# Kernel optimization log

Measured on AMD Instinct MI355X. Metric: run time of the kernel, lower is better.

Reference implementation:

```python
import jax, jax.numpy as jnp
import numpy as np

TAU = 2.0
V_TH = 1.0
V_RESET = 0.0
BN_EPS = 1e-5
SG_ALPHA = 2.0  # spikingjelly ATan surrogate default

@jax.custom_vjp
def spike_fn(x):
    return (x >= 0.0).astype(x.dtype)

def _spike_fwd(x):
    return spike_fn(x), x

def _spike_bwd(x, g):
    # ATan surrogate: alpha/2 / (1 + (pi/2*alpha*x)^2)
    sg = (SG_ALPHA / 2.0) / (1.0 + (jnp.pi / 2.0 * SG_ALPHA * x) ** 2)
    return (g * sg,)

spike_fn.defvjp(_spike_fwd, _spike_bwd)

def lif_multistep(x_seq):
    # x_seq: [T, B, C]; decay_input=False, hard reset, detach_reset=True
    def step(v, xt):
        v = v - (v - V_RESET) / TAU + xt
        s = spike_fn(v - V_TH)
        sd = jax.lax.stop_gradient(s)
        v = (1.0 - sd) * v + sd * V_RESET
        return v, s
    v0 = jnp.zeros_like(x_seq[0])
    _, s_seq = jax.lax.scan(step, v0, x_seq)
    return s_seq

def bn_eval(x, gamma, beta, mean, var):
    # x: [T, B, C], normalize over channel C (eval-mode BN)
    inv = gamma * jax.lax.rsqrt(var + BN_EPS)
    return x * inv + (beta - mean * inv)

def setup_inputs() -> dict:
    key = jax.random.key(0)
    ks = jax.random.split(key, 8)
    B, T, Cin, C, K = 64, 200, 80, 1024, 7
    x = jax.random.normal(ks[0], (B, T, Cin), dtype=jnp.float32)
    pw_w = jax.random.normal(ks[1], (C, Cin), dtype=jnp.float32) * (1.0 / np.sqrt(Cin))
    pw_b = jnp.zeros((C,), dtype=jnp.float32)
    dw_w = jax.random.normal(ks[2], (C, K), dtype=jnp.float32) * (1.0 / np.sqrt(K))
    dw_b = jnp.zeros((C,), dtype=jnp.float32)
    bn1_gamma = jnp.ones((C,), dtype=jnp.float32)
    bn1_beta = jnp.zeros((C,), dtype=jnp.float32)
    bn1_mean = jnp.zeros((C,), dtype=jnp.float32)
    bn1_var = jnp.ones((C,), dtype=jnp.float32)
    lin_w = jax.random.normal(ks[3], (C, C), dtype=jnp.float32) * (1.0 / np.sqrt(C))
    bn2_gamma = jnp.ones((C,), dtype=jnp.float32)
    bn2_beta = jnp.zeros((C,), dtype=jnp.float32)
    bn2_mean = jnp.zeros((C,), dtype=jnp.float32)
    bn2_var = jnp.ones((C,), dtype=jnp.float32)
    return dict(x=x, pw_w=pw_w, pw_b=pw_b, dw_w=dw_w, dw_b=dw_b,
                bn1_gamma=bn1_gamma, bn1_beta=bn1_beta, bn1_mean=bn1_mean, bn1_var=bn1_var,
                lin_w=lin_w,
                bn2_gamma=bn2_gamma, bn2_beta=bn2_beta, bn2_mean=bn2_mean, bn2_var=bn2_var)

def reference(x, pw_w, pw_b, dw_w, dw_b,
              bn1_gamma, bn1_beta, bn1_mean, bn1_var,
              lin_w,
              bn2_gamma, bn2_beta, bn2_mean, bn2_var):
    # x: [B, T, Cin] -> trans1 -> [B, Cin, T]
    h = jnp.transpose(x, (0, 2, 1))
    # pointwise conv1d (kernel 1): [B, Cin, T] -> [B, C, T]
    h = jnp.einsum('bct,oc->bot', h, pw_w) + pw_b[None, :, None]
    # depthwise conv1d, kernel 7, same padding
    C = dw_w.shape[0]
    h = jax.lax.conv_general_dilated(
        h, dw_w[:, None, :], window_strides=(1,), padding=[(3, 3)],
        feature_group_count=C, dimension_numbers=('NCH', 'OIH', 'NCH'))
    h = h + dw_b[None, :, None]
    # trans2: [B, C, T] -> [T, B, C]
    h = jnp.transpose(h, (2, 0, 1))
    h = bn_eval(h, bn1_gamma, bn1_beta, bn1_mean, bn1_var)
    h = lif_multistep(h)
    # dropout1: eval mode -> identity
    h_res = h
    h = jnp.einsum('tbc,oc->tbo', h, lin_w)  # Linear, no bias
    h = bn_eval(h, bn2_gamma, bn2_beta, bn2_mean, bn2_var)
    h = lif_multistep(h)
    # dropout2: eval mode -> identity
    return h + h_res  # [T, B, C]
```

## Files before the change

kernel.cpp:

```cpp
#include <hip/hip_runtime.h>
#include <hip/hip_bf16.h>
#include <stdint.h>

#define B_    64
#define T_    200
#define CIN_  80
#define C_    1024
#define M_    (B_ * T_)
#define BCEL  (B_ * C_)

typedef __attribute__((ext_vector_type(4))) float f32x4;
typedef __attribute__((ext_vector_type(8))) _Float16 f16x8;
typedef __attribute__((ext_vector_type(4))) unsigned int u32x4;

__global__ __launch_bounds__(256) void gemm_abt128(
    const float* __restrict__ A, const float* __restrict__ Bm,
    const float* __restrict__ bias, float* __restrict__ C,
    int M, int N, int K) {
  __shared__ float As[16][128];
  __shared__ float Bs[16][128];
  const int tid = threadIdx.x;
  const int tx = tid & 15;
  const int ty = tid >> 4;
  const int m0 = blockIdx.x * 128;
  const int n0 = blockIdx.y * 128;
  const int lr = tid >> 1;
  const int lc = (tid & 1) * 8;

  float acc[8][8] = {};

  const float* Ar = A + (size_t)(m0 + lr) * K + lc;
  const float* Br = Bm + (size_t)(n0 + lr) * K + lc;

  float4 a0 = *(const float4*)(Ar + 0);
  float4 a1 = *(const float4*)(Ar + 4);
  float4 b0 = *(const float4*)(Br + 0);
  float4 b1 = *(const float4*)(Br + 4);

  for (int k0 = 0; k0 < K; k0 += 16) {
    __syncthreads();
    As[lc + 0][lr] = a0.x; As[lc + 1][lr] = a0.y;
    As[lc + 2][lr] = a0.z; As[lc + 3][lr] = a0.w;
    As[lc + 4][lr] = a1.x; As[lc + 5][lr] = a1.y;
    As[lc + 6][lr] = a1.z; As[lc + 7][lr] = a1.w;
    Bs[lc + 0][lr] = b0.x; Bs[lc + 1][lr] = b0.y;
    Bs[lc + 2][lr] = b0.z; Bs[lc + 3][lr] = b0.w;
    Bs[lc + 4][lr] = b1.x; Bs[lc + 5][lr] = b1.y;
    Bs[lc + 6][lr] = b1.z; Bs[lc + 7][lr] = b1.w;
    __syncthreads();
    if (k0 + 16 < K) {
      a0 = *(const float4*)(Ar + k0 + 16);
      a1 = *(const float4*)(Ar + k0 + 20);
      b0 = *(const float4*)(Br + k0 + 16);
      b1 = *(const float4*)(Br + k0 + 20);
    }
#pragma unroll
    for (int kk = 0; kk < 16; ++kk) {
      float4 av0 = *(const float4*)&As[kk][ty * 4];
      float4 av1 = *(const float4*)&As[kk][ty * 4 + 64];
      float4 bv0 = *(const float4*)&Bs[kk][tx * 4];
      float4 bv1 = *(const float4*)&Bs[kk][tx * 4 + 64];
      float avv[8] = {av0.x, av0.y, av0.z, av0.w, av1.x, av1.y, av1.z, av1.w};
      float bvv[8] = {bv0.x, bv0.y, bv0.z, bv0.w, bv1.x, bv1.y, bv1.z, bv1.w};
#pragma unroll
      for (int i = 0; i < 8; ++i)
#pragma unroll
        for (int j = 0; j < 8; ++j)
          acc[i][j] = fmaf(avv[i], bvv[j], acc[i][j]);
    }
  }

  float bj[8] = {0.f, 0.f, 0.f, 0.f, 0.f, 0.f, 0.f, 0.f};
  if (bias) {
#pragma unroll
    for (int j = 0; j < 8; ++j)
      bj[j] = bias[n0 + tx * 4 + (j & 3) + (j >> 2) * 64];
  }
#pragma unroll
  for (int i = 0; i < 8; ++i) {
    int row = m0 + ty * 4 + (i & 3) + (i >> 2) * 64;
    float4 o0, o1;
    o0.x = acc[i][0] + bj[0]; o0.y = acc[i][1] + bj[1];
    o0.z = acc[i][2] + bj[2]; o0.w = acc[i][3] + bj[3];
    o1.x = acc[i][4] + bj[4]; o1.y = acc[i][5] + bj[5];
    o1.z = acc[i][6] + bj[6]; o1.w = acc[i][7] + bj[7];
    *(float4*)&C[(size_t)row * N + n0 + tx * 4] = o0;
    *(float4*)&C[(size_t)row * N + n0 + tx * 4 + 64] = o1;
  }
}

__global__ __launch_bounds__(256) void dw_bn_lif(
    const float* __restrict__ p, const float* __restrict__ dw_w,
    const float* __restrict__ dw_b, const float* __restrict__ gam,
    const float* __restrict__ bet, const float* __restrict__ mu,
    const float* __restrict__ var, ushort* __restrict__ s1) {
  int gid = blockIdx.x * blockDim.x + threadIdx.x;
  int b = gid >> 10;
  int o = gid & 1023;

  float w[7];
#pragma unroll
  for (int k = 0; k < 7; ++k) w[k] = dw_w[o * 7 + k];
  float db = dw_b[o];
  float inv = (float)((double)gam[o] / sqrt((double)var[o] + 1e-5));
  float add = (float)((double)bet[o] - (double)mu[o] * (double)inv);

  const float* pp = p + (size_t)b * T_ * C_ + o;
  float win[14];
  win[0] = 0.f; win[1] = 0.f; win[2] = 0.f;
#pragma unroll
  for (int i = 0; i < 11; ++i) win[3 + i] = pp[(size_t)i * C_];

  float v = 0.f;
  size_t obase = (size_t)b * C_ + o;
  for (int c = 0; c < T_ / 8; ++c) {
    int t0 = c * 8;
    float nx[8];
#pragma unroll
    for (int j = 0; j < 8; ++j) {
      int tn = t0 + 11 + j;
      nx[j] = (tn < T_) ? pp[(size_t)tn * C_] : 0.f;
    }
#pragma unroll
    for (int s = 0; s < 8; ++s) {
      float u = db;
#pragma unroll
      for (int k = 0; k < 7; ++k) u = fmaf(w[k], win[s + k], u);
      u = fmaf(u, inv, add);
      v = fmaf(0.5f, v, u);
      bool sp = (v - 1.0f) >= 0.0f;
      s1[obase + (size_t)(t0 + s) * BCEL] = sp ? (ushort)0x3C00 : (ushort)0;
      v = sp ? 0.0f : v;
    }
#pragma unroll
    for (int i = 0; i < 6; ++i) win[i] = win[i + 8];
#pragma unroll
    for (int j = 0; j < 8; ++j) win[6 + j] = nx[j];
  }
}

__global__ __launch_bounds__(256) void split_w(
    const float* __restrict__ w, ushort* __restrict__ w0,
    ushort* __restrict__ w1, int n) {
  int i = blockIdx.x * 256 + threadIdx.x;
  if (i >= n) return;
  float x = w[i];
  union { _Float16 h; ushort u; } h0, h1;
  h0.h = (_Float16)x;
  if (fabsf(x) < 6.1035156e-5f) h0.u = 0;
  float r = x - (float)h0.h;
  h1.h = (_Float16)(r * 2048.0f);
  w0[i] = h0.u;
  w1[i] = h1.u;
}

#define BM 128
#define BN 128
#define BKg 32

__global__ __launch_bounds__(256) void gemm_mfma2p(
    const ushort* __restrict__ A,
    const ushort* __restrict__ B0,
    const ushort* __restrict__ B1,
    float* __restrict__ Cout) {
  const int K = C_;
  const int N = C_;
  __shared__ __align__(16) ushort lds[2][3][BM * BKg];

  const int tid  = threadIdx.x;
  const int lane = tid & 63;
  const int wm = ((tid >> 6) >> 1) * 64;
  const int wn = ((tid >> 6) & 1) * 64;

  int lin = blockIdx.x;
  int qq = gridDim.x >> 3;
  int wg = (lin & 7) * qq + (lin >> 3);
  const int m0 = (wg >> 3) * BM;
  const int n0 = (wg & 7) * BN;

  const int r0 = tid >> 2, r1 = r0 + 64;
  const int kc = (tid & 3) * 8;
  const int ks = kc ^ (((tid >> 3) & 3) << 3);

  const int fr = lane & 15;
  const int k8 = (lane >> 4) * 8;
  const int k8s = k8 ^ (((fr >> 1) & 3) << 3);

  f32x4 acc[4][4] = {};

#define STAGE(bufi, kk0)                                                       \
  do {                                                                         \
    __builtin_amdgcn_global_load_lds(                                          \
        (const __attribute__((address_space(1))) uint32_t*)(A + (size_t)(m0 + r0) * K + (kk0) + ks),  \
        (__attribute__((address_space(3))) uint32_t*)&lds[bufi][0][tid * 8], 16, 0, 0);               \
    __builtin_amdgcn_global_load_lds(                                          \
        (const __attribute__((address_space(1))) uint32_t*)(A + (size_t)(m0 + r1) * K + (kk0) + ks),  \
        (__attribute__((address_space(3))) uint32_t*)&lds[bufi][0][(tid + 256) * 8], 16, 0, 0);       \
    __builtin_amdgcn_global_load_lds(                                          \
        (const __attribute__((address_space(1))) uint32_t*)(B0 + (size_t)(n0 + r0) * K + (kk0) + ks), \
        (__attribute__((address_space(3))) uint32_t*)&lds[bufi][1][tid * 8], 16, 0, 0);               \
    __builtin_amdgcn_global_load_lds(                                          \
        (const __attribute__((address_space(1))) uint32_t*)(B0 + (size_t)(n0 + r1) * K + (kk0) + ks), \
        (__attribute__((address_space(3))) uint32_t*)&lds[bufi][1][(tid + 256) * 8], 16, 0, 0);       \
    __builtin_amdgcn_global_load_lds(                                          \
        (const __attribute__((address_space(1))) uint32_t*)(B1 + (size_t)(n0 + r0) * K + (kk0) + ks), \
        (__attribute__((address_space(3))) uint32_t*)&lds[bufi][2][tid * 8], 16, 0, 0);               \
    __builtin_amdgcn_global_load_lds(                                          \
        (const __attribute__((address_space(1))) uint32_t*)(B1 + (size_t)(n0 + r1) * K + (kk0) + ks), \
        (__attribute__((address_space(3))) uint32_t*)&lds[bufi][2][(tid + 256) * 8], 16, 0, 0);       \
  } while (0)

  STAGE(0, 0);
  __syncthreads();

  int buf = 0;
  for (int k0 = 0; k0 < K; k0 += BKg) {
    union HU { f16x8 h; u32x4 u; };
    f16x8 af[4], a2f[4], b0f[4], b1f[4];
#pragma unroll
    for (int m = 0; m < 4; ++m) {
      HU t;
      t.h = *(const f16x8*)&lds[buf][0][(wm + m * 16 + fr) * BKg + k8s];
      af[m] = t.h;
      t.u &= 0x10001000u;
      a2f[m] = t.h;
    }
#pragma unroll
    for (int n = 0; n < 4; ++n) {
      b0f[n] = *(const f16x8*)&lds[buf][1][(wn + n * 16 + fr) * BKg + k8s];
      b1f[n] = *(const f16x8*)&lds[buf][2][(wn + n * 16 + fr) * BKg + k8s];
    }
    if (k0 + BKg < K) STAGE(buf ^ 1, k0 + BKg);
#pragma unroll
    for (int m = 0; m < 4; ++m)
#pragma unroll
      for (int n = 0; n < 4; ++n) {
        acc[m][n] = __builtin_amdgcn_mfma_f32_16x16x32_f16(
            af[m], b0f[n], acc[m][n], 0, 0, 0);
        acc[m][n] = __builtin_amdgcn_mfma_f32_16x16x32_f16(
            a2f[m], b1f[n], acc[m][n], 0, 0, 0);
      }
    __syncthreads();
    buf ^= 1;
  }
#undef STAGE

  const int ccol = lane & 15;
  const int crow = (lane >> 4) * 4;
#pragma unroll
  for (int m = 0; m < 4; ++m)
#pragma unroll
    for (int n = 0; n < 4; ++n)
#pragma unroll
      for (int j = 0; j < 4; ++j) {
        int row = m0 + wm + m * 16 + crow + j;
        int col = n0 + wn + n * 16 + ccol;
        Cout[(size_t)row * N + col] = acc[m][n][j];
      }
}

__global__ __launch_bounds__(256) void bn_lif_add(
    const float* __restrict__ y, const ushort* __restrict__ s1b,
    const float* __restrict__ gam, const float* __restrict__ bet,
    const float* __restrict__ mu, const float* __restrict__ var,
    float* __restrict__ out) {
  int gid = blockIdx.x * blockDim.x + threadIdx.x;
  int o = gid & 1023;

  float inv = (float)((double)gam[o] / sqrt((double)var[o] + 1e-5));
  float add = (float)((double)bet[o] - (double)mu[o] * (double)inv);

  float v = 0.f;
  size_t base = (size_t)gid;
  float yv[8]; ushort sv[8];
#pragma unroll
  for (int j = 0; j < 8; ++j) {
    yv[j] = y[base + (size_t)j * BCEL];
    sv[j] = s1b[base + (size_t)j * BCEL];
  }
  for (int c = 0; c < T_ / 8; ++c) {
    int t0 = c * 8;
    float yn[8] = {0,0,0,0,0,0,0,0}; ushort sn[8] = {0,0,0,0,0,0,0,0};
    if (c + 1 < T_ / 8) {
#pragma unroll
      for (int j = 0; j < 8; ++j) {
        size_t idx = base + (size_t)(t0 + 8 + j) * BCEL;
        yn[j] = y[idx];
        sn[j] = s1b[idx];
      }
    }
#pragma unroll
    for (int j = 0; j < 8; ++j) {
      float u = fmaf(yv[j], inv, add);
      v = fmaf(0.5f, v, u);
      bool sp = (v - 1.0f) >= 0.0f;
      float s1v = sv[j] ? 1.0f : 0.0f;
      out[base + (size_t)(t0 + j) * BCEL] = (sp ? 1.0f : 0.0f) + s1v;
      v = sp ? 0.0f : v;
    }
#pragma unroll
    for (int j = 0; j < 8; ++j) { yv[j] = yn[j]; sv[j] = sn[j]; }
  }
}

extern "C" void kernel_launch(void* const* d_in, const int* in_sizes, int n_in,
                              void* d_out, int out_size, void* d_ws,
                              size_t ws_size, hipStream_t stream) {
  const float* x     = (const float*)d_in[0];
  const float* pw_w  = (const float*)d_in[1];
  const float* pw_b  = (const float*)d_in[2];
  const float* dw_w  = (const float*)d_in[3];
  const float* dw_b  = (const float*)d_in[4];
  const float* bn1g  = (const float*)d_in[5];
  const float* bn1b  = (const float*)d_in[6];
  const float* bn1m  = (const float*)d_in[7];
  const float* bn1v  = (const float*)d_in[8];
  const float* lin_w = (const float*)d_in[9];
  const float* bn2g  = (const float*)d_in[10];
  const float* bn2b  = (const float*)d_in[11];
  const float* bn2m  = (const float*)d_in[12];
  const float* bn2v  = (const float*)d_in[13];

  char* wsb  = (char*)d_ws;
  char* outb = (char*)d_out;
  const size_t PB  = (size_t)M_ * C_ * 4;
  const size_t SBB = (size_t)M_ * C_ * 2;

  float* p = (float*)d_ws;

  const bool primary = ws_size >= PB + SBB;
  ushort* spikes = primary ? (ushort*)(wsb + PB) : (ushort*)d_out;
  ushort* w0  = primary ? (ushort*)outb : (ushort*)(wsb + SBB);
  ushort* w1s = w0 + (size_t)C_ * C_;
  ushort* Sgemm = primary ? spikes : (ushort*)d_ws;
  float* ybuf = primary ? (float*)d_ws : (float*)d_out;

  dim3 pw_grid(M_ / 128, C_ / 128);
  gemm_abt128<<<pw_grid, 256, 0, stream>>>(x, pw_w, pw_b, p, M_, C_, CIN_);

  dw_bn_lif<<<BCEL / 256, 256, 0, stream>>>(p, dw_w, dw_b, bn1g, bn1b, bn1m,
                                            bn1v, spikes);

  if (!primary)
    hipMemcpyAsync(d_ws, d_out, SBB, hipMemcpyDeviceToDevice, stream);

  split_w<<<(C_ * C_ + 255) / 256, 256, 0, stream>>>(lin_w, w0, w1s, C_ * C_);

  gemm_mfma2p<<<(M_ / BM) * (C_ / BN), 256, 0, stream>>>(Sgemm, w0, w1s, ybuf);

  bn_lif_add<<<BCEL / 256, 256, 0, stream>>>(ybuf, Sgemm, bn2g, bn2b, bn2m,
                                             bn2v, (float*)d_out);
}
```

Before: 153.8 us.

## Rewrite spike GEMM as 256x256 tile, 8-wave, triple-buffered phased pipeline

The split-fp16 MFMA GEMM moves from 128x128 tiles with 4 waves and double buffering to 256x256 tiles with 8 waves and a three-slot LDS ring. Each k-tile is split into four compute phases, and each phase issues the global-to-LDS loads for a future tile. Explicit barriers, vmcnt waits and s_setprio are used to overlap memory with MFMA work. The larger tile raises data reuse per load. The cost is a grid of only 200 workgroups, each using about 147KB of LDS, so the GPU may be underfilled and occupancy is limited.

```diff
diff --git a/kernel.cpp b/kernel.cpp
--- a/kernel.cpp
+++ b/kernel.cpp
@@ -154,101 +154,127 @@
   w1[i] = h1.u;
 }
 
-#define BM 128
-#define BN 128
-#define BKg 32
-
-__global__ __launch_bounds__(256) void gemm_mfma2p(
+#define GBM 256
+#define GBN 256
+#define GBK 32
+#define NKT (C_ / GBK)
+
+__global__ __launch_bounds__(512, 2) void gemm_mfma8p(
     const ushort* __restrict__ A,
     const ushort* __restrict__ B0,
     const ushort* __restrict__ B1,
     float* __restrict__ Cout) {
   const int K = C_;
   const int N = C_;
-  __shared__ __align__(16) ushort lds[2][3][BM * BKg];
+  __shared__ ushort lds8[3][3][GBM * GBK];
 
   const int tid  = threadIdx.x;
   const int lane = tid & 63;
-  const int wm = ((tid >> 6) >> 1) * 64;
-  const int wn = ((tid >> 6) & 1) * 64;
+  const int wid  = tid >> 6;
+  const int wm = (wid >> 2) * 128;
+  const int wn = (wid & 3) * 64;
 
   int lin = blockIdx.x;
-  int qq = gridDim.x >> 3;
-  int wg = (lin & 7) * qq + (lin >> 3);
-  const int m0 = (wg >> 3) * BM;
-  const int n0 = (wg & 7) * BN;
-
-  const int r0 = tid >> 2, r1 = r0 + 64;
-  const int kc = (tid & 3) * 8;
-  const int ks = kc ^ (((tid >> 3) & 3) << 3);
-
-  const int fr = lane & 15;
-  const int k8 = (lane >> 4) * 8;
-  const int k8s = k8 ^ (((fr >> 1) & 3) << 3);
-
-  f32x4 acc[4][4] = {};
-
-#define STAGE(bufi, kk0)                                                       \
+  int wg  = (lin & 7) * 25 + (lin >> 3);
+  const int m0 = (wg >> 2) * GBM;
+  const int n0 = (wg & 3) * GBN;
+
+  const int ar0 = tid >> 2, ar1 = ar0 + 128;
+  const int aks = ((tid & 3) * 8) ^ (((tid >> 3) & 3) << 3);
+
+  const int fr  = lane & 15;
+  const int k8s = ((lane >> 4) * 8) ^ (((fr >> 1) & 3) << 3);
+
+  f32x4 acc[8][4] = {};
+
+#define STG(MATP, RB, MI, SLOT, K0S)                                           \
   do {                                                                         \
     __builtin_amdgcn_global_load_lds(                                          \
-        (const __attribute__((address_space(1))) uint32_t*)(A + (size_t)(m0 + r0) * K + (kk0) + ks),  \
-        (__attribute__((address_space(3))) uint32_t*)&lds[bufi][0][tid * 8], 16, 0, 0);               \
+        (const __attribute__((address_space(1))) uint32_t*)((MATP) + (size_t)((RB) + ar0) * K + (K0S) + aks), \
+        (__attribute__((address_space(3))) uint32_t*)&lds8[SLOT][MI][tid * 8], 16, 0, 0);                     \
     __builtin_amdgcn_global_load_lds(                                          \
-        (const __attribute__((address_space(1))) uint32_t*)(A + (size_t)(m0 + r1) * K + (kk0) + ks),  \
-        (__attribute__((address_space(3))) uint32_t*)&lds[bufi][0][(tid + 256) * 8], 16, 0, 0);       \
-    __builtin_amdgcn_global_load_lds(                                          \
-        (const __attribute__((address_space(1))) uint32_t*)(B0 + (size_t)(n0 + r0) * K + (kk0) + ks), \
-        (__attribute__((address_space(3))) uint32_t*)&lds[bufi][1][tid * 8], 16, 0, 0);               \
-    __builtin_amdgcn_global_load_lds(                                          \
-        (const __attribute__((address_space(1))) uint32_t*)(B0 + (size_t)(n0 + r1) * K + (kk0) + ks), \
-        (__attribute__((address_space(3))) uint32_t*)&lds[bufi][1][(tid + 256) * 8], 16, 0, 0);       \
-    __builtin_amdgcn_global_load_lds(                                          \
-        (const __attribute__((address_space(1))) uint32_t*)(B1 + (size_t)(n0 + r0) * K + (kk0) + ks), \
-        (__attribute__((address_space(3))) uint32_t*)&lds[bufi][2][tid * 8], 16, 0, 0);               \
-    __builtin_amdgcn_global_load_lds(                                          \
-        (const __attribute__((address_space(1))) uint32_t*)(B1 + (size_t)(n0 + r1) * K + (kk0) + ks), \
-        (__attribute__((address_space(3))) uint32_t*)&lds[bufi][2][(tid + 256) * 8], 16, 0, 0);       \
+        (const __attribute__((address_space(1))) uint32_t*)((MATP) + (size_t)((RB) + ar1) * K + (K0S) + aks), \
+        (__attribute__((address_space(3))) uint32_t*)&lds8[SLOT][MI][(tid + 512) * 8], 16, 0, 0);             \
   } while (0)
 
-  STAGE(0, 0);
-  __syncthreads();
-
-  int buf = 0;
-  for (int k0 = 0; k0 < K; k0 += BKg) {
-    union HU { f16x8 h; u32x4 u; };
-    f16x8 af[4], a2f[4], b0f[4], b1f[4];
-#pragma unroll
-    for (int m = 0; m < 4; ++m) {
-      HU t;
-      t.h = *(const f16x8*)&lds[buf][0][(wm + m * 16 + fr) * BKg + k8s];
-      af[m] = t.h;
-      t.u &= 0x10001000u;
-      a2f[m] = t.h;
-    }
-#pragma unroll
-    for (int n = 0; n < 4; ++n) {
-      b0f[n] = *(const f16x8*)&lds[buf][1][(wn + n * 16 + fr) * BKg + k8s];
-      b1f[n] = *(const f16x8*)&lds[buf][2][(wn + n * 16 + fr) * BKg + k8s];
-    }
-    if (k0 + BKg < K) STAGE(buf ^ 1, k0 + BKg);
-#pragma unroll
-    for (int m = 0; m < 4; ++m)
-#pragma unroll
-      for (int n = 0; n < 4; ++n) {
-        acc[m][n] = __builtin_amdgcn_mfma_f32_16x16x32_f16(
-            af[m], b0f[n], acc[m][n], 0, 0, 0);
-        acc[m][n] = __builtin_amdgcn_mfma_f32_16x16x32_f16(
-            a2f[m], b1f[n], acc[m][n], 0, 0, 0);
-      }
-    __syncthreads();
-    buf ^= 1;
-  }
-#undef STAGE
+#define NOSTG ((void)0)
+#define VM6 asm volatile("s_waitcnt vmcnt(6)" ::: "memory")
+
+#define PHASE(Q, SRD, STAGE_STMT, VMSTMT)                                      \
+  do {                                                                         \
+    constexpr int FRB = ((Q) & 1) * 4;                                         \
+    constexpr int FCB = ((Q) >> 1) * 2;                                        \
+    const ushort* As_  = &lds8[SRD][0][0];                                     \
+    const ushort* B0s_ = &lds8[SRD][1][0];                                     \
+    const ushort* B1s_ = &lds8[SRD][2][0];                                     \
+    f16x8 a0_ = *(const f16x8*)&As_[(wm + (FRB + 0) * 16 + fr) * GBK + k8s];   \
+    f16x8 a1_ = *(const f16x8*)&As_[(wm + (FRB + 1) * 16 + fr) * GBK + k8s];   \
+    f16x8 a2_ = *(const f16x8*)&As_[(wm + (FRB + 2) * 16 + fr) * GBK + k8s];   \
+    f16x8 a3_ = *(const f16x8*)&As_[(wm + (FRB + 3) * 16 + fr) * GBK + k8s];   \
+    f16x8 p0_ = *(const f16x8*)&B0s_[(wn + (FCB + 0) * 16 + fr) * GBK + k8s];  \
+    f16x8 p1_ = *(const f16x8*)&B0s_[(wn + (FCB + 1) * 16 + fr) * GBK + k8s];  \
+    f16x8 q0_ = *(const f16x8*)&B1s_[(wn + (FCB + 0) * 16 + fr) * GBK + k8s];  \
+    f16x8 q1_ = *(const f16x8*)&B1s_[(wn + (FCB + 1) * 16 + fr) * GBK + k8s];  \
+    STAGE_STMT;                                                                \
+    __builtin_amdgcn_s_barrier();                                              \
+    asm volatile("s_waitcnt lgkmcnt(0)" ::: "memory");                         \
+    __builtin_amdgcn_s_setprio(1);                                             \
+    union HU_ { f16x8 h; u32x4 u; };                                           \
+    HU_ x0_, x1_, x2_, x3_;                                                    \
+    x0_.h = a0_; x0_.u &= 0x10001000u;                                         \
+    x1_.h = a1_; x1_.u &= 0x10001000u;                                         \
+    x2_.h = a2_; x2_.u &= 0x10001000u;                                         \
+    x3_.h = a3_; x3_.u &= 0x10001000u;                                         \
+    acc[FRB + 0][FCB + 0] = __builtin_amdgcn_mfma_f32_16x16x32_f16(a0_, p0_, acc[FRB + 0][FCB + 0], 0, 0, 0); \
+    acc[FRB + 0][FCB + 0] = __builtin_amdgcn_mfma_f32_16x16x32_f16(x0_.h, q0_, acc[FRB + 0][FCB + 0], 0, 0, 0); \
+    acc[FRB + 1][FCB + 0] = __builtin_amdgcn_mfma_f32_16x16x32_f16(a1_, p0_, acc[FRB + 1][FCB + 0], 0, 0, 0); \
+    acc[FRB + 1][FCB + 0] = __builtin_amdgcn_mfma_f32_16x16x32_f16(x1_.h, q0_, acc[FRB + 1][FCB + 0], 0, 0, 0); \
+    acc[FRB + 2][FCB + 0] = __builtin_amdgcn_mfma_f32_16x16x32_f16(a2_, p0_, acc[FRB + 2][FCB + 0], 0, 0, 0); \
+    acc[FRB + 2][FCB + 0] = __builtin_amdgcn_mfma_f32_16x16x32_f16(x2_.h, q0_, acc[FRB + 2][FCB + 0], 0, 0, 0); \
+    acc[FRB + 3][FCB + 0] = __builtin_amdgcn_mfma_f32_16x16x32_f16(a3_, p0_, acc[FRB + 3][FCB + 0], 0, 0, 0); \
+    acc[FRB + 3][FCB + 0] = __builtin_amdgcn_mfma_f32_16x16x32_f16(x3_.h, q0_, acc[FRB + 3][FCB + 0], 0, 0, 0); \
+    acc[FRB + 0][FCB + 1] = __builtin_amdgcn_mfma_f32_16x16x32_f16(a0_, p1_, acc[FRB + 0][FCB + 1], 0, 0, 0); \
+    acc[FRB + 0][FCB + 1] = __builtin_amdgcn_mfma_f32_16x16x32_f16(x0_.h, q1_, acc[FRB + 0][FCB + 1], 0, 0, 0); \
+    acc[FRB + 1][FCB + 1] = __builtin_amdgcn_mfma_f32_16x16x32_f16(a1_, p1_, acc[FRB + 1][FCB + 1], 0, 0, 0); \
+    acc[FRB + 1][FCB + 1] = __builtin_amdgcn_mfma_f32_16x16x32_f16(x1_.h, q1_, acc[FRB + 1][FCB + 1], 0, 0, 0); \
+    acc[FRB + 2][FCB + 1] = __builtin_amdgcn_mfma_f32_16x16x32_f16(a2_, p1_, acc[FRB + 2][FCB + 1], 0, 0, 0); \
+    acc[FRB + 2][FCB + 1] = __builtin_amdgcn_mfma_f32_16x16x32_f16(x2_.h, q1_, acc[FRB + 2][FCB + 1], 0, 0, 0); \
+    acc[FRB + 3][FCB + 1] = __builtin_amdgcn_mfma_f32_16x16x32_f16(a3_, p1_, acc[FRB + 3][FCB + 1], 0, 0, 0); \
+    acc[FRB + 3][FCB + 1] = __builtin_amdgcn_mfma_f32_16x16x32_f16(x3_.h, q1_, acc[FRB + 3][FCB + 1], 0, 0, 0); \
+    __builtin_amdgcn_s_setprio(0);                                             \
+    VMSTMT;                                                                    \
+    __builtin_amdgcn_s_barrier();                                              \
+  } while (0)
+
+  STG(A, m0, 0, 0, 0);  STG(B0, n0, 1, 0, 0);  STG(B1, n0, 2, 0, 0);
+  STG(A, m0, 0, 1, GBK); STG(B0, n0, 1, 1, GBK); STG(B1, n0, 2, 1, GBK);
+  asm volatile("s_waitcnt vmcnt(6)" ::: "memory");
+  __builtin_amdgcn_s_barrier();
+
+  int s0 = 0;
+  for (int it = 0; it < NKT / 2; ++it) {
+    const int t0 = 2 * it;
+    int s1 = s0 + 1; if (s1 == 3) s1 = 0;
+    int s2 = s1 + 1; if (s2 == 3) s2 = 0;
+    const int ka = (t0 + 2 < NKT) ? (t0 + 2) * GBK : 0;
+    const int kb = (t0 + 3 < NKT) ? (t0 + 3) * GBK : 0;
+    PHASE(0, s0, STG(A,  m0, 0, s2, ka), NOSTG);
+    PHASE(1, s0, STG(B0, n0, 1, s2, ka), NOSTG);
+    PHASE(2, s0, STG(B1, n0, 2, s2, ka), NOSTG);
+    PHASE(3, s0, NOSTG, VM6);
+    PHASE(0, s1, STG(A,  m0, 0, s0, kb), NOSTG);
+    PHASE(1, s1, STG(B0, n0, 1, s0, kb), NOSTG);
+    PHASE(2, s1, STG(B1, n0, 2, s0, kb), NOSTG);
+    PHASE(3, s1, NOSTG, VM6);
+    s0 = s2;
+  }
+#undef PHASE
+#undef STG
 
   const int ccol = lane & 15;
   const int crow = (lane >> 4) * 4;
 #pragma unroll
-  for (int m = 0; m < 4; ++m)
+  for (int m = 0; m < 8; ++m)
 #pragma unroll
     for (int n = 0; n < 4; ++n)
 #pragma unroll
@@ -346,7 +372,8 @@
 
   split_w<<<(C_ * C_ + 255) / 256, 256, 0, stream>>>(lin_w, w0, w1s, C_ * C_);
 
-  gemm_mfma2p<<<(M_ / BM) * (C_ / BN), 256, 0, stream>>>(Sgemm, w0, w1s, ybuf);
+  gemm_mfma8p<<<(M_ / GBM) * (C_ / GBN), 512, 0, stream>>>(Sgemm, w0, w1s,
+                                                           ybuf);
 
   bn_lif_add<<<BCEL / 256, 256, 0, stream>>>(ybuf, Sgemm, bn2g, bn2b, bn2m,
                                              bn2v, (float*)d_out);
```

After: 147.4 us. -4.2%, faster.
